# Optimization experiments

Measured on AMD Instinct MI355X. Metric: run time of the kernel, lower is better.

The kernel has to match this reference:

```python
import jax, jax.numpy as jnp
import numpy as np

HS, FF, NH = 1024, 4096, 16
HD = HS // NH
EPS = 1e-5

def _ln(x, g, b):
    m = jnp.mean(x, axis=-1, keepdims=True)
    v = jnp.mean((x - m) ** 2, axis=-1, keepdims=True)
    return (x - m) * jax.lax.rsqrt(v + EPS) * g + b

def setup_inputs() -> dict:
    key = jax.random.key(0)
    ks = jax.random.split(key, 12)
    s = 1.0 / np.sqrt(HS)
    si = 1.0 / np.sqrt(FF)
    d = {
        "hidden_states": jax.random.normal(ks[0], (2, 2048, HS), dtype=jnp.float32),
        "attention_mask": jnp.zeros((2, 1, 1, 2048), dtype=jnp.float32),
        "Wq": jax.random.uniform(ks[1], (HS, HS), minval=-s, maxval=s),
        "bq": jnp.zeros((HS,), jnp.float32),
        "Wk": jax.random.uniform(ks[2], (HS, HS), minval=-s, maxval=s),
        "bk": jnp.zeros((HS,), jnp.float32),
        "Wv": jax.random.uniform(ks[3], (HS, HS), minval=-s, maxval=s),
        "bv": jnp.zeros((HS,), jnp.float32),
        "Wo": jax.random.uniform(ks[4], (HS, HS), minval=-s, maxval=s),
        "bo": jnp.zeros((HS,), jnp.float32),
        "W1": jax.random.uniform(ks[5], (HS, FF), minval=-s, maxval=s),
        "b1": jnp.zeros((FF,), jnp.float32),
        "W2": jax.random.uniform(ks[6], (FF, HS), minval=-si, maxval=si),
        "b2": jnp.zeros((HS,), jnp.float32),
        "ln1_g": jnp.ones((HS,), jnp.float32),
        "ln1_b": jnp.zeros((HS,), jnp.float32),
        "ln2_g": jnp.ones((HS,), jnp.float32),
        "ln2_b": jnp.zeros((HS,), jnp.float32),
    }
    return d

def reference(hidden_states, attention_mask, Wq, bq, Wk, bk, Wv, bv, Wo, bo,
              W1, b1, W2, b2, ln1_g, ln1_b, ln2_g, ln2_b):
    bs, S, _ = hidden_states.shape
    x = hidden_states
    # self-attention (dropout is identity in eval)
    q = (x @ Wq + bq).reshape(bs, S, NH, HD).transpose(0, 2, 1, 3)
    k = (x @ Wk + bk).reshape(bs, S, NH, HD).transpose(0, 2, 1, 3)
    v = (x @ Wv + bv).reshape(bs, S, NH, HD).transpose(0, 2, 1, 3)
    scores = jnp.einsum("bhqd,bhkd->bhqk", q, k) / np.sqrt(HD) + attention_mask
    probs = jax.nn.softmax(scores, axis=-1)
    attn = jnp.einsum("bhqk,bhkd->bhqd", probs, v)
    attn = attn.transpose(0, 2, 1, 3).reshape(bs, S, HS)
    mha = attn @ Wo + bo
    h = _ln(x + mha, ln1_g, ln1_b)
    # FFN
    ff = jax.nn.relu(h @ W1 + b1) @ W2 + b2
    return _ln(h + ff, ln2_g, ln2_b)
```

## Files before the change

kernel.cpp:

```cpp
#include <hip/hip_runtime.h>
#include <hip/hip_bf16.h>

#define HS   1024
#define FF   4096
#define NH   16
#define HD   64
#define SEQ  2048
#define BSZ  2
#define MROWS (BSZ * SEQ)
#define EPS  1e-5f
#define QKV_STRIDE (3 * HS)

typedef float f32x4  __attribute__((ext_vector_type(4)));
typedef short bf16x8 __attribute__((ext_vector_type(8)));

#if __has_builtin(__builtin_amdgcn_exp2f)
#define EXP2(x) __builtin_amdgcn_exp2f(x)
#else
#define EXP2(x) exp2f(x)
#endif

__device__ __forceinline__ unsigned short f2bf(float x) {
  unsigned int u = __float_as_uint(x);
  u += 0x7fffu + ((u >> 16) & 1u);
  return (unsigned short)(u >> 16);
}

__device__ __forceinline__ float bf2f(unsigned short u) {
  return __uint_as_float((unsigned int)u << 16);
}

__device__ __forceinline__ unsigned int pkbf(float a, float b) {
  union { __hip_bfloat162 h; unsigned int u; } x;
  x.h = __float22bfloat162_rn(float2{a, b});
  return x.u;
}

__device__ __forceinline__ void async16(const ushort* g, ushort* lds) {
  __builtin_amdgcn_global_load_lds(
      (const __attribute__((address_space(1))) unsigned int*)g,
      (__attribute__((address_space(3))) unsigned int*)lds, 16, 0, 0);
}

#define BARSB { __builtin_amdgcn_s_barrier(); __builtin_amdgcn_sched_barrier(0); }

#define QUAD(kt, MH, NH)                                                      \
  {                                                                           \
    const ushort* As_ = &smem[(size_t)((kt) & 1) * 32768];                    \
    const ushort* Bs_ = As_ + 16384;                                          \
    bf16x8 af[4][2], bfr[2][2];                                               \
    _Pragma("unroll")                                                         \
    for (int mt = 0; mt < 4; ++mt)                                            \
      _Pragma("unroll")                                                       \
      for (int s = 0; s < 2; ++s) {                                           \
        const int m = wr * 128 + (MH) * 64 + mt * 16 + lr;                    \
        af[mt][s] = *(const bf16x8*)&As_[(size_t)m * 64 +                     \
                                         (((s * 4 + lg) ^ (m & 7)) * 8)];     \
      }                                                                       \
    _Pragma("unroll")                                                         \
    for (int nj = 0; nj < 2; ++nj)                                            \
      _Pragma("unroll")                                                       \
      for (int s = 0; s < 2; ++s) {                                           \
        const int n = wc * 64 + (NH) * 32 + nj * 16 + lr;                     \
        bfr[nj][s] = *(const bf16x8*)&Bs_[(size_t)n * 64 +                    \
                                          (((s * 4 + lg) ^ (n & 7)) * 8)];    \
      }                                                                       \
    __builtin_amdgcn_s_setprio(1);                                            \
    _Pragma("unroll")                                                         \
    for (int s = 0; s < 2; ++s)                                               \
      _Pragma("unroll")                                                       \
      for (int mt = 0; mt < 4; ++mt)                                          \
        _Pragma("unroll")                                                     \
        for (int nj = 0; nj < 2; ++nj)                                        \
          acc[(MH) * 4 + mt][(NH) * 2 + nj] =                                 \
              __builtin_amdgcn_mfma_f32_16x16x32_bf16(                        \
                  af[mt][s], bfr[nj][s], acc[(MH) * 4 + mt][(NH) * 2 + nj],   \
                  0, 0, 0);                                                   \
    __builtin_amdgcn_s_setprio(0);                                            \
  }

template <bool RELU, bool VTRANS>
__global__ __launch_bounds__(512, 2) void gemm8_bf16_kernel(
    const ushort* __restrict__ A, const ushort* __restrict__ Bt,
    const float* __restrict__ bias, ushort* __restrict__ C,
    ushort* __restrict__ VTg, int M, int N, int K)
{
  __shared__ ushort smem[65536];
  const int tid = threadIdx.x;
  const int wv = tid >> 6, ln = tid & 63;
  const int wr = wv >> 2, wc = wv & 3;
  const int lr = ln & 15, lg = ln >> 4;
  const int rr = ln >> 3, cc = ln & 7;

  const unsigned nxy = gridDim.x * gridDim.y;
  unsigned id = blockIdx.y * gridDim.x + blockIdx.x;
  id = (id & 7) * (nxy >> 3) + (id >> 3);
  const int bn = id % gridDim.x, bm = id / gridDim.x;

  f32x4 acc[8][4];
#pragma unroll
  for (int i = 0; i < 8; ++i)
#pragma unroll
    for (int j = 0; j < 4; ++j) acc[i][j] = (f32x4){0.f, 0.f, 0.f, 0.f};

  auto stA = [&](int kt, int h) {
#pragma unroll
    for (int u = 0; u < 2; ++u) {
      const int tt = h + u * 2;
      const int R = tt * 64 + wv * 8 + rr;
      async16(A + (size_t)(bm * 256 + R) * K + kt * 64 + ((cc ^ (R & 7)) * 8),
              &smem[(size_t)(kt & 1) * 32768 + (size_t)(tt * 64 + wv * 8) * 64]);
    }
  };
  auto stB = [&](int kt, int h) {
#pragma unroll
    for (int u = 0; u < 2; ++u) {
      const int tt = h * 2 + u;
      const int R = tt * 64 + wv * 8 + rr;
      async16(Bt + (size_t)(bn * 256 + R) * K + kt * 64 + ((cc ^ (R & 7)) * 8),
              &smem[(size_t)(kt & 1) * 32768 + 16384 + (size_t)(tt * 64 + wv * 8) * 64]);
    }
  };

  stA(0, 0); stA(0, 1); stB(0, 0); stB(0, 1); stA(1, 0);

  const int nIter = K >> 7;
  for (int j = 0; j < nIter; ++j) {
    const int t0 = 2 * j, t1 = t0 + 1;
    const bool nx = (j + 1 < nIter);
    BARSB;
    stA(t1, 1);
    asm volatile("s_waitcnt vmcnt(4)" ::: "memory");
    BARSB;
    QUAD(t0, 0, 0);
    BARSB; stB(t1, 0); QUAD(t0, 0, 1);
    BARSB; if (nx) stA(t0 + 2, 0); QUAD(t0, 1, 0);
    BARSB; stB(t1, 1); QUAD(t0, 1, 1);
    BARSB;
    if (nx) {
      stA(t0 + 2, 1);
      asm volatile("s_waitcnt vmcnt(2)" ::: "memory");
    } else {
      asm volatile("s_waitcnt vmcnt(0)" ::: "memory");
    }
    BARSB;
    QUAD(t1, 0, 0);
    BARSB; if (nx) stB(t0 + 2, 0); QUAD(t1, 0, 1);
    BARSB; if (nx) stB(t0 + 2, 1); QUAD(t1, 1, 0);
    BARSB; if (nx) stA(t0 + 3, 0); QUAD(t1, 1, 1);
  }

  const int gm0 = bm * 256 + wr * 128;
  const int gn0 = bn * 256 + wc * 64;
  float bs4[4];
#pragma unroll
  for (int j = 0; j < 4; ++j) bs4[j] = bias[gn0 + j * 16 + lr];

  if (VTRANS && gn0 >= 2 * HS) {
#pragma unroll
    for (int i = 0; i < 8; ++i) {
#pragma unroll
      for (int j = 0; j < 4; ++j) {
        const int col = gn0 - 2 * HS + j * 16 + lr;
        const int rowb = gm0 + i * 16 + lg * 4;
        const int bb = rowb >> 11;
        const int seq = rowb & (SEQ - 1);
        ushort4 o;
        o.x = f2bf(acc[i][j][0] + bs4[j]);
        o.y = f2bf(acc[i][j][1] + bs4[j]);
        o.z = f2bf(acc[i][j][2] + bs4[j]);
        o.w = f2bf(acc[i][j][3] + bs4[j]);
        *(ushort4*)&VTg[((size_t)(bb * NH + (col >> 6)) * 64 + (col & 63)) * SEQ + seq] = o;
      }
    }
  } else {
#pragma unroll
    for (int i = 0; i < 8; ++i) {
#pragma unroll
      for (int r = 0; r < 4; ++r) {
        const size_t row = (size_t)(gm0 + i * 16 + lg * 4 + r);
#pragma unroll
        for (int j = 0; j < 4; ++j) {
          float val = acc[i][j][r] + bs4[j];
          if (RELU) val = fmaxf(val, 0.f);
          C[row * N + gn0 + j * 16 + lr] = f2bf(val);
        }
      }
    }
  }
}

template <int TBM, int TBN, bool RELU, bool OUT_BF16, bool PARTIAL>
__global__ __launch_bounds__(256) void gemm_bf16_kernel(
    const ushort* __restrict__ A, const ushort* __restrict__ Bt,
    const float* __restrict__ bias, void* __restrict__ Cout,
    int M, int N, int K, int kLen, size_t zstride)
{
  constexpr int MI = TBM / 32;
  constexpr int NJ = TBN / 32;
  __shared__ ushort As[TBM * 64];
  __shared__ ushort Bs[TBN * 64];

  const int tid = threadIdx.x;
  const int wv = tid >> 6, ln = tid & 63;

  const unsigned nxy = gridDim.x * gridDim.y;
  unsigned id = blockIdx.y * gridDim.x + blockIdx.x;
  id = (id & 7) * (nxy >> 3) + (id >> 3);
  const int bn = id % gridDim.x, bm = id / gridDim.x;

  const int lr = ln & 15;
  const int lg = ln >> 4;
  const int mrow_base = (wv >> 1) * (TBM / 2);
  const int ncol_base = (wv & 1) * (TBN / 2);

  f32x4 acc[MI][NJ];
#pragma unroll
  for (int i = 0; i < MI; ++i)
#pragma unroll
    for (int j = 0; j < NJ; ++j) acc[i][j] = (f32x4){0.f, 0.f, 0.f, 0.f};

  const int rr = ln >> 3, cc = ln & 7;
  const int kBeg = blockIdx.z * kLen, kEnd = kBeg + kLen;

  for (int k0 = kBeg; k0 < kEnd; k0 += 64) {
    __syncthreads();
#pragma unroll
    for (int t = 0; t < TBM / 32; ++t) {
      const int R = wv * (TBM / 4) + t * 8 + rr;
      const int c = cc ^ (R & 7);
      async16(A + (size_t)(bm * TBM + R) * K + k0 + c * 8,
              &As[(size_t)(wv * (TBM / 4) + t * 8) * 64]);
    }
#pragma unroll
    for (int t = 0; t < TBN / 32; ++t) {
      const int R = wv * (TBN / 4) + t * 8 + rr;
      const int c = cc ^ (R & 7);
      async16(Bt + (size_t)(bn * TBN + R) * K + k0 + c * 8,
              &Bs[(size_t)(wv * (TBN / 4) + t * 8) * 64]);
    }
    __syncthreads();

#pragma unroll
    for (int s = 0; s < 2; ++s) {
      bf16x8 a[MI], b[NJ];
#pragma unroll
      for (int i = 0; i < MI; ++i) {
        const int m = mrow_base + i * 16 + lr;
        a[i] = *(const bf16x8*)&As[(size_t)m * 64 + (((s * 4 + lg) ^ (m & 7)) * 8)];
      }
#pragma unroll
      for (int j = 0; j < NJ; ++j) {
        const int n = ncol_base + j * 16 + lr;
        b[j] = *(const bf16x8*)&Bs[(size_t)n * 64 + (((s * 4 + lg) ^ (n & 7)) * 8)];
      }
#pragma unroll
      for (int i = 0; i < MI; ++i)
#pragma unroll
        for (int j = 0; j < NJ; ++j)
          acc[i][j] = __builtin_amdgcn_mfma_f32_16x16x32_bf16(a[i], b[j], acc[i][j], 0, 0, 0);
    }
  }

  const int gm0 = bm * TBM + mrow_base;
  const int gn0 = bn * TBN + ncol_base;

  if (PARTIAL) {
    float* Cp = (float*)Cout + (size_t)blockIdx.z * zstride;
#pragma unroll
    for (int i = 0; i < MI; ++i)
#pragma unroll
      for (int r = 0; r < 4; ++r) {
        const size_t row = (size_t)(gm0 + i * 16 + lg * 4 + r);
#pragma unroll
        for (int j = 0; j < NJ; ++j)
          Cp[row * N + gn0 + j * 16 + lr] = acc[i][j][r];
      }
  } else {
    float bs4[NJ];
#pragma unroll
    for (int j = 0; j < NJ; ++j) bs4[j] = bias[gn0 + j * 16 + lr];
    float* Cf = (float*)Cout;
    ushort* Cb = (ushort*)Cout;
#pragma unroll
    for (int i = 0; i < MI; ++i) {
#pragma unroll
      for (int r = 0; r < 4; ++r) {
        const size_t row = (size_t)(gm0 + i * 16 + lg * 4 + r);
#pragma unroll
        for (int j = 0; j < NJ; ++j) {
          float val = acc[i][j][r] + bs4[j];
          if (RELU) val = fmaxf(val, 0.f);
          const size_t idx = row * N + gn0 + j * 16 + lr;
          if (OUT_BF16) Cb[idx] = f2bf(val);
          else          Cf[idx] = val;
        }
      }
    }
  }
}

__device__ __forceinline__ void transpose_tile(
    const float* __restrict__ W, ushort* __restrict__ Wt,
    int K, int N, int n0, int k0, int tid, ushort (*T)[72])
{
#pragma unroll
  for (int t = 0; t < 4; ++t) {
    const int r = t * 16 + (tid >> 4);
    const int c = (tid & 15) * 4;
    const float4 w = *(const float4*)&W[(size_t)(k0 + r) * N + n0 + c];
    T[c + 0][r] = f2bf(w.x); T[c + 1][r] = f2bf(w.y);
    T[c + 2][r] = f2bf(w.z); T[c + 3][r] = f2bf(w.w);
  }
  __syncthreads();
#pragma unroll
  for (int t = 0; t < 4; ++t) {
    const int n = t * 16 + (tid >> 4);
    const int kc = (tid & 15) * 4;
    ushort4 o;
    o.x = T[n][kc]; o.y = T[n][kc + 1]; o.z = T[n][kc + 2]; o.w = T[n][kc + 3];
    *(ushort4*)&Wt[(size_t)(n0 + n) * K + k0 + kc] = o;
  }
}

__global__ __launch_bounds__(256) void prep_kernel(
    const float* __restrict__ Wq, const float* __restrict__ Wk,
    const float* __restrict__ Wv, const float* __restrict__ Wo,
    const float* __restrict__ W1, const float* __restrict__ W2,
    const float* __restrict__ bq, const float* __restrict__ bk,
    const float* __restrict__ bv, const float* __restrict__ x,
    const float* __restrict__ mask,
    ushort* __restrict__ Wqkvt, ushort* __restrict__ Wot,
    ushort* __restrict__ W1t, ushort* __restrict__ W2t,
    float* __restrict__ bqkv, ushort* __restrict__ xb,
    float* __restrict__ maskL2)
{
  __shared__ ushort T[64][72];
  const int b = blockIdx.x, tid = threadIdx.x;
  const size_t M1 = 1024 * 1024;
  if (b < 1024) {
    const int w = b >> 8, l = b & 255;
    const int n0 = (l & 15) * 64, k0 = (l >> 4) * 64;
    const float* src = (w == 0) ? Wq : (w == 1) ? Wk : (w == 2) ? Wv : Wo;
    ushort* dst = (w < 3) ? (Wqkvt + (size_t)w * M1) : Wot;
    transpose_tile(src, dst, HS, HS, n0, k0, tid, T);
  } else if (b < 2048) {
    const int l = b - 1024;
    transpose_tile(W1, W1t, HS, FF, (l & 63) * 64, (l >> 6) * 64, tid, T);
  } else if (b < 3072) {
    const int l = b - 2048;
    transpose_tile(W2, W2t, FF, HS, (l & 15) * 64, (l >> 4) * 64, tid, T);
  } else if (b < 5120) {
    const size_t base = (size_t)(b - 3072) * 2048 + tid * 8;
    const float4 v0 = *(const float4*)&x[base];
    const float4 v1 = *(const float4*)&x[base + 4];
    ushort4 o0, o1;
    o0.x = f2bf(v0.x); o0.y = f2bf(v0.y); o0.z = f2bf(v0.z); o0.w = f2bf(v0.w);
    o1.x = f2bf(v1.x); o1.y = f2bf(v1.y); o1.z = f2bf(v1.z); o1.w = f2bf(v1.w);
    *(ushort4*)&xb[base] = o0;
    *(ushort4*)&xb[base + 4] = o1;
  } else {
#pragma unroll
    for (int t = 0; t < 12; ++t) {
      const int i = t * 256 + tid;
      bqkv[i] = (i < HS) ? bq[i] : (i < 2 * HS) ? bk[i - HS] : bv[i - 2 * HS];
    }
#pragma unroll
    for (int t = 0; t < 16; ++t) {
      const int i = t * 256 + tid;
      maskL2[i] = mask[i] * 1.44269504f;
    }
  }
}

__global__ __launch_bounds__(512, 2) void attention_mfma_kernel(
    const ushort* __restrict__ Qb, const ushort* __restrict__ Kb,
    const ushort* __restrict__ VTg, const float* __restrict__ maskL2,
    ushort* __restrict__ O)
{
  __shared__ ushort smem[69632];
  float* mL = (float*)(smem + 65536);

  const int tid = threadIdx.x;
  const int wv = tid >> 6, ln = tid & 63;
  const int c = ln & 15, g = ln >> 4;

  const unsigned d0 = blockIdx.x + 8u * (blockIdx.y + 16u * blockIdx.z);
  const unsigned w0 = (d0 & 7) * 32 + (d0 >> 3);
  const int qt = w0 & 7;
  const int hh = (w0 >> 3) & 15;
  const int b  = w0 >> 7;

  const int bh = b * NH + hh;
  const size_t row0 = (size_t)b * SEQ + (size_t)qt * 256;
  const int ch = hh * HD;
  const int wq0 = wv * 32;

  bf16x8 qf[2][2];
#pragma unroll
  for (int nt = 0; nt < 2; ++nt)
#pragma unroll
    for (int s = 0; s < 2; ++s)
      qf[nt][s] = *(const bf16x8*)&Qb[(row0 + wq0 + nt * 16 + c) * QKV_STRIDE + ch + s * 32 + g * 8];

  const float* mrow = maskL2 + (size_t)b * SEQ;
  async16((const ushort*)(mrow + wv * 256 + ln * 4), (ushort*)(mL + wv * 256));

  const int rr = ln >> 3, cc = ln & 7;
  const int r4 = ln >> 4, sc = ln & 15;

  auto stage = [&](int kb, int bsel) {
    ushort* Ks  = smem + bsel * 16384;
    ushort* VTs = Ks + 8192;
    const size_t krow0 = (size_t)b * SEQ + (size_t)kb * 128;
#pragma unroll
    for (int t = 0; t < 2; ++t) {
      const int r = wv * 16 + t * 8 + rr;
      async16(Kb + (krow0 + r) * QKV_STRIDE + ch + ((cc ^ (r & 7)) * 8),
              &Ks[(size_t)(wv * 16 + t * 8) * 64]);
    }
#pragma unroll
    for (int t = 0; t < 2; ++t) {
      const int d = wv * 8 + t * 4 + r4;
      const int srcc = (sc & 8) | ((sc & 7) ^ (d & 7));
      async16(VTg + ((size_t)bh * 64 + d) * SEQ + kb * 128 + srcc * 8,
              &VTs[(size_t)(wv * 8 + t * 4) * 128]);
    }
  };

  f32x4 ao[4][2];
#pragma unroll
  for (int i = 0; i < 4; ++i) { ao[i][0] = (f32x4){0,0,0,0}; ao[i][1] = (f32x4){0,0,0,0}; }
  f32x4 aol[2];
  aol[0] = (f32x4){0,0,0,0}; aol[1] = (f32x4){0,0,0,0};
  const short oneb = (short)0x3F80;
  const bf16x8 ones = (bf16x8){oneb, oneb, oneb, oneb, oneb, oneb, oneb, oneb};

  stage(0, 0);
  stage(1, 1);

  constexpr int NT = SEQ / 128;
  for (int kb = 0; kb < NT; ++kb) {
    const int cur = kb & 3;
    if (kb + 2 < NT) stage(kb + 2, (kb + 2) & 3);
    if (kb + 2 < NT)      asm volatile("s_waitcnt vmcnt(8)" ::: "memory");
    else if (kb + 1 < NT) asm volatile("s_waitcnt vmcnt(4)" ::: "memory");
    else                  asm volatile("s_waitcnt vmcnt(0)" ::: "memory");
    __builtin_amdgcn_s_barrier();
    __builtin_amdgcn_sched_barrier(0);

    ushort* Ks  = smem + cur * 16384;
    ushort* VTs = Ks + 8192;

    f32x4 asA[4][2], asB[4][2];
#pragma unroll
    for (int i = 0; i < 4; ++i) {
      asA[i][0] = (f32x4){0,0,0,0}; asA[i][1] = (f32x4){0,0,0,0};
      asB[i][0] = (f32x4){0,0,0,0}; asB[i][1] = (f32x4){0,0,0,0};
    }
    __builtin_amdgcn_s_setprio(1);
#pragma unroll
    for (int s = 0; s < 2; ++s) {
#pragma unroll
      for (int mt = 0; mt < 4; ++mt) {
        const int key = mt * 16 + c;
        const bf16x8 kf = *(const bf16x8*)&Ks[(size_t)key * 64 + (((s * 4 + g) ^ (key & 7)) * 8)];
#pragma unroll
        for (int nt = 0; nt < 2; ++nt)
          asA[mt][nt] = __builtin_amdgcn_mfma_f32_16x16x32_bf16(kf, qf[nt][s], asA[mt][nt], 0, 0, 0);
      }
    }
#pragma unroll
    for (int s = 0; s < 2; ++s) {
#pragma unroll
      for (int mt = 0; mt < 4; ++mt) {
        const int key = (mt + 4) * 16 + c;
        const bf16x8 kf = *(const bf16x8*)&Ks[(size_t)key * 64 + (((s * 4 + g) ^ (key & 7)) * 8)];
#pragma unroll
        for (int nt = 0; nt < 2; ++nt)
          asB[mt][nt] = __builtin_amdgcn_mfma_f32_16x16x32_bf16(kf, qf[nt][s], asB[mt][nt], 0, 0, 0);
      }
    }
    __builtin_amdgcn_s_setprio(0);

#pragma unroll
    for (int mt = 0; mt < 4; ++mt) {
      const float4 mk = *(const float4*)&mL[kb * 128 + mt * 16 + g * 4];
      const float mka[4] = {mk.x, mk.y, mk.z, mk.w};
#pragma unroll
      for (int nt = 0; nt < 2; ++nt) {
#pragma unroll
        for (int r = 0; r < 4; ++r)
          asA[mt][nt][r] = EXP2(fmaf(asA[mt][nt][r], 0.18033688f, mka[r]));
      }
    }

#pragma unroll
    for (int s = 0; s < 2; ++s) {
      bf16x8 pf[2];
#pragma unroll
      for (int nt = 0; nt < 2; ++nt) {
        const unsigned A0 = pkbf(asA[2 * s][nt][0], asA[2 * s][nt][1]);
        const unsigned A1 = pkbf(asA[2 * s][nt][2], asA[2 * s][nt][3]);
        const unsigned B0 = pkbf(asA[2 * s + 1][nt][0], asA[2 * s + 1][nt][1]);
        const unsigned B1 = pkbf(asA[2 * s + 1][nt][2], asA[2 * s + 1][nt][3]);
        auto x0 = __builtin_amdgcn_permlane32_swap(A0, B0, false, false);
        auto x1 = __builtin_amdgcn_permlane32_swap(A1, B1, false, false);
        auto y0 = __builtin_amdgcn_permlane16_swap(x0[0], x0[1], false, false);
        auto y1 = __builtin_amdgcn_permlane16_swap(x1[0], x1[1], false, false);
        union { unsigned w[4]; bf16x8 v; } u;
        u.w[0] = y0[0]; u.w[1] = y1[0]; u.w[2] = y0[1]; u.w[3] = y1[1];
        pf[nt] = u.v;
      }
      __builtin_amdgcn_s_setprio(1);
#pragma unroll
      for (int mt = 0; mt < 4; ++mt) {
        const int d = mt * 16 + c;
        const int k = s * 4 + g;
        const int vslot = (k & 8) | ((k & 7) ^ (d & 7));
        const bf16x8 vf = *(const bf16x8*)&VTs[(size_t)d * 128 + vslot * 8];
#pragma unroll
        for (int nt = 0; nt < 2; ++nt)
          ao[mt][nt] = __builtin_amdgcn_mfma_f32_16x16x32_bf16(vf, pf[nt], ao[mt][nt], 0, 0, 0);
      }
#pragma unroll
      for (int nt = 0; nt < 2; ++nt)
        aol[nt] = __builtin_amdgcn_mfma_f32_16x16x32_bf16(ones, pf[nt], aol[nt], 0, 0, 0);
      __builtin_amdgcn_s_setprio(0);
    }

#pragma unroll
    for (int mt = 0; mt < 4; ++mt) {
      const float4 mk = *(const float4*)&mL[kb * 128 + (mt + 4) * 16 + g * 4];
      const float mka[4] = {mk.x, mk.y, mk.z, mk.w};
#pragma unroll
      for (int nt = 0; nt < 2; ++nt) {
#pragma unroll
        for (int r = 0; r < 4; ++r)
          asB[mt][nt][r] = EXP2(fmaf(asB[mt][nt][r], 0.18033688f, mka[r]));
      }
    }

#pragma unroll
    for (int s = 2; s < 4; ++s) {
      const int sb = s - 2;
      bf16x8 pf[2];
#pragma unroll
      for (int nt = 0; nt < 2; ++nt) {
        const unsigned A0 = pkbf(asB[2 * sb][nt][0], asB[2 * sb][nt][1]);
        const unsigned A1 = pkbf(asB[2 * sb][nt][2], asB[2 * sb][nt][3]);
        const unsigned B0 = pkbf(asB[2 * sb + 1][nt][0], asB[2 * sb + 1][nt][1]);
        const unsigned B1 = pkbf(asB[2 * sb + 1][nt][2], asB[2 * sb + 1][nt][3]);
        auto x0 = __builtin_amdgcn_permlane32_swap(A0, B0, false, false);
        auto x1 = __builtin_amdgcn_permlane32_swap(A1, B1, false, false);
        auto y0 = __builtin_amdgcn_permlane16_swap(x0[0], x0[1], false, false);
        auto y1 = __builtin_amdgcn_permlane16_swap(x1[0], x1[1], false, false);
        union { unsigned w[4]; bf16x8 v; } u;
        u.w[0] = y0[0]; u.w[1] = y1[0]; u.w[2] = y0[1]; u.w[3] = y1[1];
        pf[nt] = u.v;
      }
      __builtin_amdgcn_s_setprio(1);
#pragma unroll
      for (int mt = 0; mt < 4; ++mt) {
        const int d = mt * 16 + c;
        const int k = s * 4 + g;
        const int vslot = (k & 8) | ((k & 7) ^ (d & 7));
        const bf16x8 vf = *(const bf16x8*)&VTs[(size_t)d * 128 + vslot * 8];
#pragma unroll
        for (int nt = 0; nt < 2; ++nt)
          ao[mt][nt] = __builtin_amdgcn_mfma_f32_16x16x32_bf16(vf, pf[nt], ao[mt][nt], 0, 0, 0);
      }
#pragma unroll
      for (int nt = 0; nt < 2; ++nt)
        aol[nt] = __builtin_amdgcn_mfma_f32_16x16x32_bf16(ones, pf[nt], aol[nt], 0, 0, 0);
      __builtin_amdgcn_s_setprio(0);
    }
  }

  __syncthreads();
  ushort* OL = smem;
#pragma unroll
  for (int nt = 0; nt < 2; ++nt) {
    const float inv = 1.f / aol[nt][0];
    const int q = wq0 + nt * 16 + c;
#pragma unroll
    for (int mt = 0; mt < 4; ++mt) {
      const int d = mt * 16 + g * 4;
      uint2 w;
      w.x = pkbf(ao[mt][nt][0] * inv, ao[mt][nt][1] * inv);
      w.y = pkbf(ao[mt][nt][2] * inv, ao[mt][nt][3] * inv);
      *(uint2*)&OL[q * 72 + d] = w;
    }
  }
  __syncthreads();
#pragma unroll
  for (int it = 0; it < 4; ++it) {
    const int unit = it * 512 + tid;
    const int q = unit >> 3, sg = unit & 7;
    const uint4 w = *(const uint4*)&OL[q * 72 + sg * 8];
    *(uint4*)&O[(row0 + q) * HS + ch + sg * 8] = w;
  }
}

template <bool EMIT16>
__global__ __launch_bounds__(256) void add_ln_red_kernel(
    const float* __restrict__ P0, const float* __restrict__ P1,
    const float* __restrict__ bias, const float* __restrict__ X,
    const float* __restrict__ g, const float* __restrict__ b,
    float* __restrict__ out, ushort* __restrict__ outb)
{
  const int row = blockIdx.x;
  const int tid = threadIdx.x;
  const size_t base = (size_t)row * HS + tid * 4;
  const float4 p0 = *(const float4*)&P0[base];
  const float4 p1 = *(const float4*)&P1[base];
  const float4 bi = *(const float4*)&bias[tid * 4];
  const float4 xv = *(const float4*)&X[base];
  float4 v;
  v.x = xv.x + p0.x + p1.x + bi.x;
  v.y = xv.y + p0.y + p1.y + bi.y;
  v.z = xv.z + p0.z + p1.z + bi.z;
  v.w = xv.w + p0.w + p1.w + bi.w;
  float s1 = v.x + v.y + v.z + v.w;
  float s2 = v.x * v.x + v.y * v.y + v.z * v.z + v.w * v.w;
#pragma unroll
  for (int off = 32; off > 0; off >>= 1) {
    s1 += __shfl_down(s1, off, 64);
    s2 += __shfl_down(s2, off, 64);
  }
  __shared__ float red[8];
  __shared__ float stat[2];
  const int wid = tid >> 6;
  if ((tid & 63) == 0) { red[wid] = s1; red[4 + wid] = s2; }
  __syncthreads();
  if (tid == 0) {
    const float t1 = red[0] + red[1] + red[2] + red[3];
    const float t2 = red[4] + red[5] + red[6] + red[7];
    const float mean = t1 * (1.f / HS);
    const float var = t2 * (1.f / HS) - mean * mean;
    stat[0] = mean;
    stat[1] = rsqrtf(var + EPS);
  }
  __syncthreads();
  const float mean = stat[0], rstd = stat[1];
  const float4 gv = *(const float4*)&g[tid * 4];
  const float4 bv = *(const float4*)&b[tid * 4];
  float4 r;
  r.x = (v.x - mean) * rstd * gv.x + bv.x;
  r.y = (v.y - mean) * rstd * gv.y + bv.y;
  r.z = (v.z - mean) * rstd * gv.z + bv.z;
  r.w = (v.w - mean) * rstd * gv.w + bv.w;
  *(float4*)&out[base] = r;
  if (EMIT16) {
    ushort4 o;
    o.x = f2bf(r.x); o.y = f2bf(r.y); o.z = f2bf(r.z); o.w = f2bf(r.w);
    *(ushort4*)&outb[base] = o;
  }
}

__global__ __launch_bounds__(256) void add_ln_bf16_kernel(
    const ushort* __restrict__ Pb, const float* __restrict__ X,
    const float* __restrict__ g, const float* __restrict__ b,
    float* __restrict__ out, ushort* __restrict__ outb)
{
  const int row = blockIdx.x;
  const int tid = threadIdx.x;
  const size_t base = (size_t)row * HS + tid * 4;
  const ushort4 pb = *(const ushort4*)&Pb[base];
  const float4 xv = *(const float4*)&X[base];
  float4 v;
  v.x = xv.x + bf2f(pb.x);
  v.y = xv.y + bf2f(pb.y);
  v.z = xv.z + bf2f(pb.z);
  v.w = xv.w + bf2f(pb.w);
  float s1 = v.x + v.y + v.z + v.w;
  float s2 = v.x * v.x + v.y * v.y + v.z * v.z + v.w * v.w;
#pragma unroll
  for (int off = 32; off > 0; off >>= 1) {
    s1 += __shfl_down(s1, off, 64);
    s2 += __shfl_down(s2, off, 64);
  }
  __shared__ float red[8];
  __shared__ float stat[2];
  const int wid = tid >> 6;
  if ((tid & 63) == 0) { red[wid] = s1; red[4 + wid] = s2; }
  __syncthreads();
  if (tid == 0) {
    const float t1 = red[0] + red[1] + red[2] + red[3];
    const float t2 = red[4] + red[5] + red[6] + red[7];
    const float mean = t1 * (1.f / HS);
    const float var = t2 * (1.f / HS) - mean * mean;
    stat[0] = mean;
    stat[1] = rsqrtf(var + EPS);
  }
  __syncthreads();
  const float mean = stat[0], rstd = stat[1];
  const float4 gv = *(const float4*)&g[tid * 4];
  const float4 bv = *(const float4*)&b[tid * 4];
  float4 r;
  r.x = (v.x - mean) * rstd * gv.x + bv.x;
  r.y = (v.y - mean) * rstd * gv.y + bv.y;
  r.z = (v.z - mean) * rstd * gv.z + bv.z;
  r.w = (v.w - mean) * rstd * gv.w + bv.w;
  *(float4*)&out[base] = r;
  ushort4 o;
  o.x = f2bf(r.x); o.y = f2bf(r.y); o.z = f2bf(r.z); o.w = f2bf(r.w);
  *(ushort4*)&outb[base] = o;
}

extern "C" void kernel_launch(void* const* d_in, const int* in_sizes, int n_in,
                              void* d_out, int out_size, void* d_ws, size_t ws_size,
                              hipStream_t stream)
{
  const float* x    = (const float*)d_in[0];
  const float* mask = (const float*)d_in[1];
  const float* Wq   = (const float*)d_in[2];  const float* bq  = (const float*)d_in[3];
  const float* Wk   = (const float*)d_in[4];  const float* bk  = (const float*)d_in[5];
  const float* Wv   = (const float*)d_in[6];  const float* bv  = (const float*)d_in[7];
  const float* Wo   = (const float*)d_in[8];  const float* bo  = (const float*)d_in[9];
  const float* W1   = (const float*)d_in[10]; const float* b1  = (const float*)d_in[11];
  const float* W2   = (const float*)d_in[12]; const float* b2  = (const float*)d_in[13];
  const float* g1   = (const float*)d_in[14]; const float* be1 = (const float*)d_in[15];
  const float* g2   = (const float*)d_in[16]; const float* be2 = (const float*)d_in[17];
  float* out = (float*)d_out;

  ushort* wsu = (ushort*)d_ws;
  const size_t M1 = 1024 * 1024;

  ushort* Wqkvt = wsu;
  ushort* Wot   = wsu + 3 * M1;
  ushort* W1t   = wsu + 4 * M1;
  ushort* W2t   = wsu + 8 * M1;
  float*  bqkv  = (float*)(wsu + 12 * M1);
  float*  maskL2= (float*)(wsu + 12 * M1 + 8192);
  ushort* xb    = wsu + 13 * M1;
  ushort* qkvb  = wsu + 17 * M1;
  ushort* VTg   = wsu + 29 * M1;
  ushort* attnb = wsu + 33 * M1;
  ushort* mhab  = wsu + 13 * M1;
  float*  h     = (float*)(wsu + 29 * M1);
  ushort* hb    = wsu + 37 * M1;
  ushort* ff1o  = wsu + 13 * M1;
  float*  ff2P0 = (float*)wsu;
  float*  ff2P1 = (float*)(wsu + 39 * M1);

  const dim3 blk(256);

  prep_kernel<<<dim3(5121), blk, 0, stream>>>(
      Wq, Wk, Wv, Wo, W1, W2, bq, bk, bv, x, mask,
      Wqkvt, Wot, W1t, W2t, bqkv, xb, maskL2);

  gemm8_bf16_kernel<false, true><<<dim3(12, 16), dim3(512), 0, stream>>>(
      xb, Wqkvt, bqkv, qkvb, VTg, MROWS, 3 * HS, HS);

  attention_mfma_kernel<<<dim3(SEQ / 256, NH, BSZ), dim3(512), 0, stream>>>(
      qkvb, qkvb + HS, VTg, maskL2, attnb);

  gemm_bf16_kernel<64, 128, false, true, false><<<dim3(8, 64), blk, 0, stream>>>(
      attnb, Wot, bo, mhab, MROWS, HS, HS, HS, 0);
  add_ln_bf16_kernel<<<dim3(MROWS), blk, 0, stream>>>(
      mhab, x, g1, be1, h, hb);

  gemm8_bf16_kernel<true, false><<<dim3(16, 16), dim3(512), 0, stream>>>(
      hb, W1t, b1, ff1o, nullptr, MROWS, FF, HS);

  gemm_bf16_kernel<128, 128, false, false, true><<<dim3(8, 32, 2), blk, 0, stream>>>(
      ff1o, W2t, nullptr, ff2P0, MROWS, HS, FF, FF / 2, (size_t)(ff2P1 - ff2P0));
  add_ln_red_kernel<false><<<dim3(MROWS), blk, 0, stream>>>(
      ff2P0, ff2P1, b2, h, g2, be2, out, nullptr);
}
```

Before: 335.4 us.

## Run FF2 GEMM on the 256x256 pipelined kernel with 3-way split-K

Adds a PARTIAL mode to the 256x256 pipelined gemm8 kernel. Each z-slice covers a K range and writes raw fp32 partial sums to its own buffer. The second FFN GEMM moves to this kernel with a 3-way K split (1408/1408/1280), replacing the 128x128 tile kernel with a 2-way split. The reduction+LayerNorm kernel now sums three partials, and one partial reuses the output buffer as scratch. The aim is more operand reuse per block and a faster main loop, at the cost of only 192 large blocks (possibly underfilling the CUs) and an extra partial buffer to read and write.

```diff
diff --git a/kernel.cpp b/kernel.cpp
--- a/kernel.cpp
+++ b/kernel.cpp
@@ -79,11 +79,13 @@
     __builtin_amdgcn_s_setprio(0);                                            \
   }
 
-template <bool RELU, bool VTRANS>
+template <bool RELU, bool VTRANS, bool PARTIAL>
 __global__ __launch_bounds__(512, 2) void gemm8_bf16_kernel(
     const ushort* __restrict__ A, const ushort* __restrict__ Bt,
     const float* __restrict__ bias, ushort* __restrict__ C,
-    ushort* __restrict__ VTg, int M, int N, int K)
+    ushort* __restrict__ VTg,
+    float* __restrict__ P0, float* __restrict__ P1, float* __restrict__ P2,
+    int M, int N, int K, int kSplit)
 {
   __shared__ ushort smem[65536];
   const int tid = threadIdx.x;
@@ -97,6 +99,13 @@
   id = (id & 7) * (nxy >> 3) + (id >> 3);
   const int bn = id % gridDim.x, bm = id / gridDim.x;
 
+  int kBeg = 0, kEnd = K;
+  if (PARTIAL) {
+    kBeg = blockIdx.z * kSplit;
+    kEnd = kBeg + kSplit; if (kEnd > K) kEnd = K;
+  }
+  const int jBeg = kBeg >> 7, jEnd = kEnd >> 7;
+
   f32x4 acc[8][4];
 #pragma unroll
   for (int i = 0; i < 8; ++i)
@@ -122,12 +131,12 @@
     }
   };
 
-  stA(0, 0); stA(0, 1); stB(0, 0); stB(0, 1); stA(1, 0);
-
-  const int nIter = K >> 7;
-  for (int j = 0; j < nIter; ++j) {
+  const int tP = 2 * jBeg;
+  stA(tP, 0); stA(tP, 1); stB(tP, 0); stB(tP, 1); stA(tP + 1, 0);
+
+  for (int j = jBeg; j < jEnd; ++j) {
     const int t0 = 2 * j, t1 = t0 + 1;
-    const bool nx = (j + 1 < nIter);
+    const bool nx = (j + 1 < jEnd);
     BARSB;
     stA(t1, 1);
     asm volatile("s_waitcnt vmcnt(4)" ::: "memory");
@@ -152,6 +161,22 @@
 
   const int gm0 = bm * 256 + wr * 128;
   const int gn0 = bn * 256 + wc * 64;
+
+  if (PARTIAL) {
+    float* Cp = (blockIdx.z == 0) ? P0 : (blockIdx.z == 1) ? P1 : P2;
+#pragma unroll
+    for (int i = 0; i < 8; ++i) {
+#pragma unroll
+      for (int r = 0; r < 4; ++r) {
+        const size_t row = (size_t)(gm0 + i * 16 + lg * 4 + r);
+#pragma unroll
+        for (int j = 0; j < 4; ++j)
+          Cp[row * N + gn0 + j * 16 + lr] = acc[i][j][r];
+      }
+    }
+    return;
+  }
+
   float bs4[4];
 #pragma unroll
   for (int j = 0; j < 4; ++j) bs4[j] = bias[gn0 + j * 16 + lr];
@@ -602,25 +627,26 @@
   }
 }
 
-template <bool EMIT16>
-__global__ __launch_bounds__(256) void add_ln_red_kernel(
+__global__ __launch_bounds__(256) void add_ln_red3_kernel(
     const float* __restrict__ P0, const float* __restrict__ P1,
+    const float* __restrict__ P2,
     const float* __restrict__ bias, const float* __restrict__ X,
     const float* __restrict__ g, const float* __restrict__ b,
-    float* __restrict__ out, ushort* __restrict__ outb)
+    float* __restrict__ out)
 {
   const int row = blockIdx.x;
   const int tid = threadIdx.x;
   const size_t base = (size_t)row * HS + tid * 4;
   const float4 p0 = *(const float4*)&P0[base];
   const float4 p1 = *(const float4*)&P1[base];
+  const float4 p2 = *(const float4*)&P2[base];
   const float4 bi = *(const float4*)&bias[tid * 4];
   const float4 xv = *(const float4*)&X[base];
   float4 v;
-  v.x = xv.x + p0.x + p1.x + bi.x;
-  v.y = xv.y + p0.y + p1.y + bi.y;
-  v.z = xv.z + p0.z + p1.z + bi.z;
-  v.w = xv.w + p0.w + p1.w + bi.w;
+  v.x = xv.x + p0.x + p1.x + p2.x + bi.x;
+  v.y = xv.y + p0.y + p1.y + p2.y + bi.y;
+  v.z = xv.z + p0.z + p1.z + p2.z + bi.z;
+  v.w = xv.w + p0.w + p1.w + p2.w + bi.w;
   float s1 = v.x + v.y + v.z + v.w;
   float s2 = v.x * v.x + v.y * v.y + v.z * v.z + v.w * v.w;
 #pragma unroll
@@ -651,11 +677,6 @@
   r.z = (v.z - mean) * rstd * gv.z + bv.z;
   r.w = (v.w - mean) * rstd * gv.w + bv.w;
   *(float4*)&out[base] = r;
-  if (EMIT16) {
-    ushort4 o;
-    o.x = f2bf(r.x); o.y = f2bf(r.y); o.z = f2bf(r.z); o.w = f2bf(r.w);
-    *(ushort4*)&outb[base] = o;
-  }
 }
 
 __global__ __launch_bounds__(256) void add_ln_bf16_kernel(
@@ -742,7 +763,8 @@
   ushort* hb    = wsu + 37 * M1;
   ushort* ff1o  = wsu + 13 * M1;
   float*  ff2P0 = (float*)wsu;
-  float*  ff2P1 = (float*)(wsu + 39 * M1);
+  float*  ff2P1 = (float*)(wsu + 37 * M1);
+  float*  ff2P2 = out;
 
   const dim3 blk(256);
 
@@ -750,8 +772,8 @@
       Wq, Wk, Wv, Wo, W1, W2, bq, bk, bv, x, mask,
       Wqkvt, Wot, W1t, W2t, bqkv, xb, maskL2);
 
-  gemm8_bf16_kernel<false, true><<<dim3(12, 16), dim3(512), 0, stream>>>(
-      xb, Wqkvt, bqkv, qkvb, VTg, MROWS, 3 * HS, HS);
+  gemm8_bf16_kernel<false, true, false><<<dim3(12, 16), dim3(512), 0, stream>>>(
+      xb, Wqkvt, bqkv, qkvb, VTg, nullptr, nullptr, nullptr, MROWS, 3 * HS, HS, 0);
 
   attention_mfma_kernel<<<dim3(SEQ / 256, NH, BSZ), dim3(512), 0, stream>>>(
       qkvb, qkvb + HS, VTg, maskL2, attnb);
@@ -761,11 +783,12 @@
   add_ln_bf16_kernel<<<dim3(MROWS), blk, 0, stream>>>(
       mhab, x, g1, be1, h, hb);
 
-  gemm8_bf16_kernel<true, false><<<dim3(16, 16), dim3(512), 0, stream>>>(
-      hb, W1t, b1, ff1o, nullptr, MROWS, FF, HS);
-
-  gemm_bf16_kernel<128, 128, false, false, true><<<dim3(8, 32, 2), blk, 0, stream>>>(
-      ff1o, W2t, nullptr, ff2P0, MROWS, HS, FF, FF / 2, (size_t)(ff2P1 - ff2P0));
-  add_ln_red_kernel<false><<<dim3(MROWS), blk, 0, stream>>>(
-      ff2P0, ff2P1, b2, h, g2, be2, out, nullptr);
-}
+  gemm8_bf16_kernel<true, false, false><<<dim3(16, 16), dim3(512), 0, stream>>>(
+      hb, W1t, b1, ff1o, nullptr, nullptr, nullptr, nullptr, MROWS, FF, HS, 0);
+
+  gemm8_bf16_kernel<false, false, true><<<dim3(4, 16, 3), dim3(512), 0, stream>>>(
+      ff1o, W2t, nullptr, nullptr, nullptr, ff2P0, ff2P1, ff2P2,
+      MROWS, HS, FF, 1408);
+  add_ln_red3_kernel<<<dim3(MROWS), blk, 0, stream>>>(
+      ff2P0, ff2P1, ff2P2, b2, h, g2, be2, out);
+}
```

Measured after the change: 332.7 us, median of 2. No clear change (-0.8%).
